# Optimization experiments

Measured on AMD Instinct MI355X. Metric: run time of the kernel, lower is better.

Reference implementation:

```python
import jax, jax.numpy as jnp
import numpy as np

HEADS = 20
DIM_HEAD = 64


def _bicubic_matrix(out_size, in_size, a=-0.75):
    """Separable torch-style bicubic (align_corners=False, antialias=False) as a [out,in] matrix."""
    W = np.zeros((out_size, in_size), dtype=np.float32)
    scale = in_size / out_size
    for i in range(out_size):
        x = (i + 0.5) * scale - 0.5
        x0 = int(np.floor(x))
        t = x - x0
        for tap, dist in zip(range(-1, 3), (1.0 + t, t, 1.0 - t, 2.0 - t)):
            d = abs(dist)
            if d <= 1.0:
                w = (a + 2.0) * d**3 - (a + 3.0) * d**2 + 1.0
            elif d < 2.0:
                w = a * d**3 - 5.0 * a * d**2 + 8.0 * a * d - 4.0 * a
            else:
                w = 0.0
            W[i, min(max(x0 + tap, 0), in_size - 1)] += w
    return jnp.asarray(W)


def setup_inputs() -> dict:
    key = jax.random.key(0)
    ks = jax.random.split(key, 8)
    B, N, QD, CD = 8, 4096, 1280, 1024
    inner = HEADS * DIM_HEAD
    return {
        "x": jax.random.normal(ks[0], (B, N, QD), dtype=jnp.float32),
        "context": jax.random.normal(ks[1], (B, 85, CD), dtype=jnp.float32),
        "Wq": jax.random.normal(ks[2], (QD, inner), dtype=jnp.float32) * 0.02,
        "Wk": jax.random.normal(ks[3], (CD, inner), dtype=jnp.float32) * 0.02,
        "Wv": jax.random.normal(ks[4], (CD, inner), dtype=jnp.float32) * 0.02,
        "Wo": jax.random.normal(ks[5], (inner, QD), dtype=jnp.float32) * 0.02,
        "bo": jnp.zeros((QD,), dtype=jnp.float32),
        "mask": jax.random.randint(ks[6], (B, 1, 256, 256), 0, 2, dtype=jnp.int32),
    }


def reference(x, context, Wq, Wk, Wv, Wo, bo, mask):
    B, N, _ = x.shape
    h, d = HEADS, DIM_HEAD
    scale = d ** -0.5
    q = (x @ Wq).reshape(B, N, h, d)
    k = (context @ Wk).reshape(B, -1, h, d)
    v = (context @ Wv).reshape(B, -1, h, d)
    # fp32 QK^T as in _ATTN_PRECISION == 'fp32'
    sim = jnp.einsum('bihd,bjhd->bhij', q.astype(jnp.float32), k.astype(jnp.float32)) * scale
    # build custom mask: bicubic-resize fg map to hw x hw, threshold, tile x4, append bg, prepend 77 ones
    hw = int(round(N ** 0.5))
    R = _bicubic_matrix(hw, mask.shape[-1])  # [hw, Hin]
    mf = mask.astype(jnp.float32)  # [B,1,H,W]
    resized = jnp.einsum('oh,bchw,pw->bcop', R, mf, R)  # [B,1,hw,hw]
    fg = (resized != 0).transpose(0, 2, 3, 1).reshape(B, hw * hw, 1)  # b (h w) c
    fg = jnp.repeat(fg, 4, axis=-1)  # b i (j k), k=4
    bg = ~fg
    base = jnp.ones((B, hw * hw, 77), dtype=bool)
    m = jnp.concatenate([base, fg, bg], axis=-1)  # [B, N, 85]
    neg = -jnp.finfo(sim.dtype).max
    sim = jnp.where(m[:, None, :, :], sim, neg)
    attn = jax.nn.softmax(sim, axis=-1)
    out = jnp.einsum('bhij,bjhd->bihd', attn.astype(v.dtype), v).reshape(B, N, h * d)
    return out @ Wo + bo
```

## Files before the change

kernel.cpp:

```cpp
#include <hip/hip_runtime.h>
#include <math.h>

typedef _Float16 f16;
typedef _Float16 half8 __attribute__((ext_vector_type(8)));
typedef _Float16 half4v __attribute__((ext_vector_type(4)));
typedef float f32x4 __attribute__((ext_vector_type(4)));

#define NB 8
#define SEQ 4096
#define QDIM 1280
#define CDIM 1024
#define INNER 1280
#define CTX 85
#define CTXP 96

#define VMCNT(n) asm volatile("s_waitcnt vmcnt(" #n ")" ::: "memory")
#define BAR() do { asm volatile("" ::: "memory"); __builtin_amdgcn_s_barrier(); asm volatile("" ::: "memory"); } while (0)

__device__ __forceinline__ void gload16(const void* g, void* l) {
  __builtin_amdgcn_global_load_lds(
      (const __attribute__((address_space(1))) unsigned int*)g,
      (__attribute__((address_space(3))) unsigned int*)l, 16, 0, 0);
}

__global__ void k_cast(const float* __restrict__ x, f16* __restrict__ xh, long n8) {
  long i = blockIdx.x * 256L + threadIdx.x;
  if (i >= n8) return;
  float4 a = ((const float4*)x)[2 * i];
  float4 b = ((const float4*)x)[2 * i + 1];
  half8 o;
  o[0] = (f16)a.x; o[1] = (f16)a.y; o[2] = (f16)a.z; o[3] = (f16)a.w;
  o[4] = (f16)b.x; o[5] = (f16)b.y; o[6] = (f16)b.z; o[7] = (f16)b.w;
  *(half8*)(xh + 8 * i) = o;
}

__global__ void k_castctx(const float* __restrict__ ctx, f16* __restrict__ ctxh) {
  int id = blockIdx.x * 256 + threadIdx.x;
  int b = id / (96 * 128);
  int rem = id % (96 * 128);
  int j = rem >> 7;
  int kc = (rem & 127) * 8;
  half8 o = {};
  if (j < CTX) {
    const float* p = ctx + ((long)b * CTX + j) * CDIM + kc;
    float4 a = *(const float4*)p;
    float4 c = *(const float4*)(p + 4);
    o[0] = (f16)a.x; o[1] = (f16)a.y; o[2] = (f16)a.z; o[3] = (f16)a.w;
    o[4] = (f16)c.x; o[5] = (f16)c.y; o[6] = (f16)c.z; o[7] = (f16)c.w;
  }
  *(half8*)(ctxh + (long)id * 8) = o;
}

__global__ __launch_bounds__(256) void k_transpose(const float* __restrict__ in,
                                                   f16* __restrict__ out, int K, int Nn) {
  __shared__ __attribute__((aligned(16))) f16 T[64][72];
  int n0 = blockIdx.x * 64, k0 = blockIdx.y * 64;
  int t = threadIdx.x;
  int kr = t >> 4, nc = (t & 15) * 4;
  for (int i = 0; i < 4; i++) {
    int k = kr + i * 16;
    float4 v = *(const float4*)&in[(long)(k0 + k) * Nn + n0 + nc];
    T[nc + 0][k] = (f16)v.x;
    T[nc + 1][k] = (f16)v.y;
    T[nc + 2][k] = (f16)v.z;
    T[nc + 3][k] = (f16)v.w;
  }
  __syncthreads();
  for (int i = 0; i < 2; i++) {
    int slot = t + i * 256;
    int n = slot >> 3, ch = (slot & 7) * 8;
    *(half8*)&out[(long)(n0 + n) * K + k0 + ch] = *(half8*)&T[n][ch];
  }
}

__global__ void k_fg(const int* __restrict__ mask, unsigned char* __restrict__ fg) {
  int id = blockIdx.x * 256 + threadIdx.x;
  int b = id >> 12, o = (id >> 6) & 63, p = id & 63;
  const int* mb = mask + (long)b * 65536;
  const int w[4] = {-3, 19, 19, -3};
  int s = 0;
  for (int dh = 0; dh < 4; dh++) {
    const int* row = mb + (4 * o + dh) * 256 + 4 * p;
    int rs = -3 * row[0] + 19 * row[1] + 19 * row[2] - 3 * row[3];
    s += w[dh] * rs;
  }
  fg[id] = (s != 0) ? 1 : 0;
}

__global__ __launch_bounds__(256) void k_kvproj(const f16* __restrict__ ctxh,
    const f16* __restrict__ WkT, const f16* __restrict__ WvT,
    f16* __restrict__ kpad, f16* __restrict__ vT) {
  int b = blockIdx.y, kv = blockIdx.z;
  const f16* WT = kv ? WvT : WkT;
  int w = threadIdx.x >> 6, lane = threadIdx.x & 63;
  int ln = lane & 15, qd = lane >> 4;
  int n0 = (blockIdx.x * 4 + w) * 16;
  const f16* arow = ctxh + ((long)b * CTXP + ln) * CDIM + qd * 8;
  const f16* brow = WT + (long)(n0 + ln) * CDIM + qd * 8;
  f32x4 acc[6] = {};
#pragma unroll 4
  for (int k0 = 0; k0 < CDIM; k0 += 32) {
    half8 bf = *(const half8*)(brow + k0);
#pragma unroll
    for (int mt = 0; mt < 6; mt++) {
      half8 af = *(const half8*)(arow + mt * 16 * CDIM + k0);
      acc[mt] = __builtin_amdgcn_mfma_f32_16x16x32_f16(af, bf, acc[mt], 0, 0, 0);
    }
  }
  if (kv == 0) {
    for (int mt = 0; mt < 6; mt++)
      for (int r = 0; r < 4; r++)
        kpad[((long)b * CTXP + mt * 16 + qd * 4 + r) * INNER + n0 + ln] = (f16)acc[mt][r];
  } else {
    for (int mt = 0; mt < 6; mt++) {
      half4v pv;
      for (int r = 0; r < 4; r++) pv[r] = (f16)acc[mt][r];
      *(half4v*)&vT[((long)b * INNER + n0 + ln) * CTXP + mt * 16 + qd * 4] = pv;
    }
  }
}

template <int OUT_F32>
__global__ __launch_bounds__(256) void k_gemm(const f16* __restrict__ A,
    const f16* __restrict__ Bt, const float* __restrict__ bias,
    f16* __restrict__ outh, float* __restrict__ outf, int K) {
  __shared__ __attribute__((aligned(16))) f16 Alds[128 * 64];
  __shared__ __attribute__((aligned(16))) f16 Blds[128 * 64];
  int tid = threadIdx.x, lane = tid & 63, w = tid >> 6;
  int wr = w >> 1, wc = w & 1;
  int ln = lane & 15, qd = lane >> 4;
  long m0 = (long)blockIdx.x * 128;
  int n0 = blockIdx.y * 128;
  int srow = lane >> 3;
  int schunk = lane & 7;
  f32x4 acc[4][4] = {};
  for (int k0 = 0; k0 < K; k0 += 64) {
#pragma unroll
    for (int i = 0; i < 4; i++) {
      int row = w * 32 + i * 8 + srow;
      int ca = (schunk ^ (row & 7)) * 8;
      gload16(&A[(m0 + row) * K + k0 + ca], &Alds[w * 2048 + i * 512]);
      gload16(&Bt[(long)(n0 + row) * K + k0 + ca], &Blds[w * 2048 + i * 512]);
    }
    __syncthreads();
#pragma unroll
    for (int s = 0; s < 2; s++) {
      half8 af[4], bf[4];
#pragma unroll
      for (int mt = 0; mt < 4; mt++) {
        int row = wr * 64 + mt * 16 + ln;
        af[mt] = *(half8*)&Alds[row * 64 + (((s * 4 + qd) ^ (row & 7)) * 8)];
      }
#pragma unroll
      for (int nt = 0; nt < 4; nt++) {
        int row = wc * 64 + nt * 16 + ln;
        bf[nt] = *(half8*)&Blds[row * 64 + (((s * 4 + qd) ^ (row & 7)) * 8)];
      }
#pragma unroll
      for (int mt = 0; mt < 4; mt++)
#pragma unroll
        for (int nt = 0; nt < 4; nt++)
          acc[mt][nt] = __builtin_amdgcn_mfma_f32_16x16x32_f16(af[mt], bf[nt], acc[mt][nt], 0, 0, 0);
    }
    __syncthreads();
  }
  for (int mt = 0; mt < 4; mt++) {
    long mrow = m0 + wr * 64 + mt * 16 + qd * 4;
    for (int nt = 0; nt < 4; nt++) {
      int n = n0 + wc * 64 + nt * 16 + ln;
      float bv = OUT_F32 ? bias[n] : 0.f;
      for (int r = 0; r < 4; r++) {
        if (OUT_F32) outf[(mrow + r) * INNER + n] = acc[mt][nt][r] + bv;
        else         outh[(mrow + r) * INNER + n] = (f16)acc[mt][nt][r];
      }
    }
  }
}

__device__ __forceinline__ void stage2(const f16* __restrict__ g, int ldK,
                                       f16* lds, int tid, int c0) {
#pragma unroll
  for (int c = c0; c < c0 + 2; ++c) {
    int row = c * 64 + (tid >> 3);
    int sc = (tid & 7) ^ (row & 7);
    gload16(g + (long)row * ldK + sc * 8, lds + c * 4096 + (tid >> 6) * 512);
  }
}

template <int OUT_F32>
__global__ __launch_bounds__(512, 2) void k_gemm256(const f16* __restrict__ A,
    const f16* __restrict__ Bt, const float* __restrict__ bias,
    f16* __restrict__ outh, float* __restrict__ outf, int K) {
  extern __shared__ __attribute__((aligned(16))) f16 smem[];
  f16* As0 = smem;
  f16* As1 = smem + 16384;
  f16* Bs0 = smem + 32768;
  f16* Bs1 = smem + 49152;
  const int NT = K >> 6;
  int tid = threadIdx.x, lane = tid & 63, w = tid >> 6;
  int wr = w >> 2, wc = w & 3;
  int ln = lane & 15, qd = lane >> 4;
  int wrb = wr * 128, wcb = wc * 64;
  int cpx = gridDim.x >> 3;
  int swz = (blockIdx.x & 7) * cpx + (blockIdx.x >> 3);
  int mtile = swz & 127, ntile = swz >> 7;
  long m0 = (long)mtile * 256;
  int n0 = ntile * 256;
  const f16* Ab = A + m0 * K;
  const f16* Bb = Bt + (long)n0 * K;

  half8 af[4][2], bf[2][2];
  f32x4 acc[8][4] = {};

  auto rdA = [&](const f16* Ac, int mh) {
#pragma unroll
    for (int mt = 0; mt < 4; ++mt) {
      int R = wrb + mh * 64 + mt * 16 + ln;
      const f16* rp = Ac + R * 64;
      int r7 = (R & 7) << 3;
      af[mt][0] = *(const half8*)(rp + ((qd << 3) ^ r7));
      af[mt][1] = *(const half8*)(rp + (((4 + qd) << 3) ^ r7));
    }
  };
  auto rdB = [&](const f16* Bc, int nh) {
#pragma unroll
    for (int nt = 0; nt < 2; ++nt) {
      int R = wcb + nh * 32 + nt * 16 + ln;
      const f16* rp = Bc + R * 64;
      int r7 = (R & 7) << 3;
      bf[nt][0] = *(const half8*)(rp + ((qd << 3) ^ r7));
      bf[nt][1] = *(const half8*)(rp + (((4 + qd) << 3) ^ r7));
    }
  };
  auto mm = [&](int mh, int nh) {
    __builtin_amdgcn_s_setprio(1);
#pragma unroll
    for (int ks = 0; ks < 2; ++ks)
#pragma unroll
      for (int mt = 0; mt < 4; ++mt)
#pragma unroll
        for (int nt = 0; nt < 2; ++nt)
          acc[mh * 4 + mt][nh * 2 + nt] = __builtin_amdgcn_mfma_f32_16x16x32_f16(
              af[mt][ks], bf[nt][ks], acc[mh * 4 + mt][nh * 2 + nt], 0, 0, 0);
    __builtin_amdgcn_s_setprio(0);
  };

  stage2(Ab, K, As0, tid, 0); stage2(Ab, K, As0, tid, 2);
  stage2(Bb, K, Bs0, tid, 0); stage2(Bb, K, Bs0, tid, 2);
  if (NT > 1) { stage2(Ab + 64, K, As1, tid, 0); VMCNT(2); } else { VMCNT(0); }
  BAR();

#define TILE256(KT, AC, BC, AN, BN_) do {                                        \
    rdA(AC, 0); rdB(BC, 0);                                                      \
    if ((KT) + 1 < NT) { stage2(Ab + ((KT) + 1) * 64, K, AN, tid, 2);            \
                         stage2(Bb + ((KT) + 1) * 64, K, BN_, tid, 0); }         \
    BAR(); mm(0, 0); BAR();                                                      \
    rdB(BC, 1);                                                                  \
    if ((KT) + 1 < NT) stage2(Bb + ((KT) + 1) * 64, K, BN_, tid, 2);             \
    BAR(); mm(0, 1); BAR();                                                      \
    rdA(AC, 1);                                                                  \
    BAR(); mm(1, 1); BAR();                                                      \
    rdB(BC, 0);                                                                  \
    if ((KT) + 2 < NT) stage2(Ab + ((KT) + 2) * 64, K, AC, tid, 0);              \
    BAR(); mm(1, 0);                                                             \
    if ((KT) + 2 < NT) { VMCNT(2); } else if ((KT) + 1 < NT) { VMCNT(0); }       \
    BAR();                                                                       \
  } while (0)

#pragma unroll 1
  for (int kt = 0; kt < NT; kt += 2) {
    TILE256(kt, As0, Bs0, As1, Bs1);
    TILE256(kt + 1, As1, Bs1, As0, Bs0);
  }
#undef TILE256

#pragma unroll
  for (int mt = 0; mt < 8; ++mt) {
    long rb = m0 + wrb + mt * 16 + qd * 4;
#pragma unroll
    for (int nt = 0; nt < 4; ++nt) {
      int col = n0 + wcb + nt * 16 + ln;
      if (OUT_F32) {
        float bv = bias[col];
#pragma unroll
        for (int r = 0; r < 4; ++r)
          outf[(rb + r) * INNER + col] = acc[mt][nt][r] + bv;
      } else {
#pragma unroll
        for (int r = 0; r < 4; ++r)
          outh[(rb + r) * INNER + col] = (f16)acc[mt][nt][r];
      }
    }
  }
}

__global__ __launch_bounds__(256) void k_attn(const f16* __restrict__ q,
    const f16* __restrict__ kpad, const f16* __restrict__ vT,
    const unsigned char* __restrict__ fg, f16* __restrict__ ao) {
  int mb = blockIdx.x;
  int h = blockIdx.y;
  int b = blockIdx.z;
  __shared__ __attribute__((aligned(16))) f16 Klds[CTXP][72];
  __shared__ __attribute__((aligned(16))) f16 Vlds[64][104];
  __shared__ __attribute__((aligned(16))) f16 Plds[4][16][104];
  int tid = threadIdx.x, lane = tid & 63, w = tid >> 6;
  int ln = lane & 15, qd = lane >> 4;

  for (int c = tid; c < CTXP * 8; c += 256) {
    int j = c >> 3, kc = (c & 7) * 8;
    *(half8*)&Klds[j][kc] = *(const half8*)&kpad[((long)b * CTXP + j) * INNER + h * 64 + kc];
  }
  for (int c = tid; c < 64 * 12; c += 256) {
    int d = c / 12, jc = (c % 12) * 8;
    *(half8*)&Vlds[d][jc] = *(const half8*)&vT[((long)b * INNER + h * 64 + d) * CTXP + jc];
  }
  __syncthreads();

  long mg = (long)b * SEQ + mb * 64 + w * 16 + ln;
  half8 qf[2];
  for (int s = 0; s < 2; s++)
    qf[s] = *(const half8*)&q[mg * INNER + h * 64 + s * 32 + qd * 8];

  f32x4 sacc[6] = {};
  for (int s = 0; s < 2; s++)
    for (int nt = 0; nt < 6; nt++) {
      half8 bf = *(half8*)&Klds[nt * 16 + ln][s * 32 + qd * 8];
      sacc[nt] = __builtin_amdgcn_mfma_f32_16x16x32_f16(qf[s], bf, sacc[nt], 0, 0, 0);
    }

  unsigned int fgw = *(const unsigned int*)&fg[(long)b * SEQ + mb * 64 + w * 16 + qd * 4];
  const float scale = 0.125f;
  for (int r = 0; r < 4; r++) {
    bool f = ((fgw >> (8 * r)) & 0xff) != 0;
    float vals[6];
    bool oks[6];
    float mx = -1e30f;
    for (int nt = 0; nt < 6; nt++) {
      int j = nt * 16 + ln;
      bool ok = (j < 77) || (j < 81 ? f : (j < 85 ? !f : false));
      float v = sacc[nt][r] * scale;
      vals[nt] = v; oks[nt] = ok;
      if (ok) mx = fmaxf(mx, v);
    }
    for (int d = 1; d < 16; d <<= 1) mx = fmaxf(mx, __shfl_xor(mx, d, 64));
    float sum = 0.f, p[6];
    for (int nt = 0; nt < 6; nt++) {
      p[nt] = oks[nt] ? __expf(vals[nt] - mx) : 0.f;
      sum += p[nt];
    }
    for (int d = 1; d < 16; d <<= 1) sum += __shfl_xor(sum, d, 64);
    float inv = 1.f / sum;
    for (int nt = 0; nt < 6; nt++)
      Plds[w][qd * 4 + r][nt * 16 + ln] = (f16)(p[nt] * inv);
  }
  __syncthreads();

  f32x4 oacc[4] = {};
  for (int ks = 0; ks < 3; ks++) {
    half8 pf = *(half8*)&Plds[w][ln][ks * 32 + qd * 8];
    for (int ntd = 0; ntd < 4; ntd++) {
      half8 vf = *(half8*)&Vlds[ntd * 16 + ln][ks * 32 + qd * 8];
      oacc[ntd] = __builtin_amdgcn_mfma_f32_16x16x32_f16(pf, vf, oacc[ntd], 0, 0, 0);
    }
  }
  for (int ntd = 0; ntd < 4; ntd++)
    for (int r = 0; r < 4; r++)
      Plds[w][qd * 4 + r][ntd * 16 + ln] = (f16)oacc[ntd][r];
  __syncthreads();
  long rowbase = (long)b * SEQ + mb * 64 + w * 16;
  for (int i = 0; i < 2; i++) {
    int slot = lane + i * 64;
    int rrow = slot >> 3, ch = (slot & 7) * 8;
    *(half8*)&ao[(rowbase + rrow) * INNER + h * 64 + ch] = *(half8*)&Plds[w][rrow][ch];
  }
}

extern "C" void kernel_launch(void* const* d_in, const int* in_sizes, int n_in,
                              void* d_out, int out_size, void* d_ws, size_t ws_size,
                              hipStream_t stream) {
  const float* x   = (const float*)d_in[0];
  const float* ctx = (const float*)d_in[1];
  const float* Wq  = (const float*)d_in[2];
  const float* Wk  = (const float*)d_in[3];
  const float* Wv  = (const float*)d_in[4];
  const float* Wo  = (const float*)d_in[5];
  const float* bo  = (const float*)d_in[6];
  const int*  mask = (const int*)d_in[7];
  float* out = (float*)d_out;

  char* ws = (char*)d_ws;
  size_t off = 0;
  f16* xh  = (f16*)(ws + off); off += 83886080;
  f16* q   = (f16*)(ws + off); off += 83886080;
  f16* ao  = (f16*)(ws + off); off += 83886080;
  f16* WqT = (f16*)(ws + off); off += 3276800;
  f16* WoT = (f16*)(ws + off); off += 3276800;
  f16* WkT = (f16*)(ws + off); off += 2621440;
  f16* WvT = (f16*)(ws + off); off += 2621440;
  f16* kpad= (f16*)(ws + off); off += 1966080;
  f16* vT  = (f16*)(ws + off); off += 1966080;
  f16* ctxh= (f16*)(ws + off); off += 1572864;
  unsigned char* fg = (unsigned char*)(ws + off); off += 32768;
  if (ws_size < off) return;

  static int g_use256 = -1;
  if (g_use256 < 0) {
    auto* f0 = k_gemm256<0>;
    auto* f1 = k_gemm256<1>;
    hipError_t e0 = hipFuncSetAttribute(reinterpret_cast<const void*>(f0),
                                        hipFuncAttributeMaxDynamicSharedMemorySize, 131072);
    hipError_t e1 = hipFuncSetAttribute(reinterpret_cast<const void*>(f1),
                                        hipFuncAttributeMaxDynamicSharedMemorySize, 131072);
    g_use256 = (e0 == hipSuccess && e1 == hipSuccess) ? 1 : 0;
  }

  k_cast<<<20480, 256, 0, stream>>>(x, xh, 5242880);
  k_castctx<<<384, 256, 0, stream>>>(ctx, ctxh);
  k_transpose<<<dim3(1280/64, 1280/64), 256, 0, stream>>>(Wq, WqT, 1280, 1280);
  k_transpose<<<dim3(1280/64, 1024/64), 256, 0, stream>>>(Wk, WkT, 1024, 1280);
  k_transpose<<<dim3(1280/64, 1024/64), 256, 0, stream>>>(Wv, WvT, 1024, 1280);
  k_transpose<<<dim3(1280/64, 1280/64), 256, 0, stream>>>(Wo, WoT, 1280, 1280);
  k_fg<<<128, 256, 0, stream>>>(mask, fg);
  k_kvproj<<<dim3(20, 8, 2), 256, 0, stream>>>(ctxh, WkT, WvT, kpad, vT);
  if (g_use256) {
    k_gemm256<0><<<640, 512, 131072, stream>>>(xh, WqT, nullptr, q, nullptr, 1280);
  } else {
    k_gemm<0><<<dim3(256, 10), 256, 0, stream>>>(xh, WqT, nullptr, q, nullptr, 1280);
  }
  k_attn<<<dim3(64, 20, 8), 256, 0, stream>>>(q, kpad, vT, fg, ao);
  if (g_use256) {
    k_gemm256<1><<<640, 512, 131072, stream>>>(ao, WoT, bo, nullptr, out, 1280);
  } else {
    k_gemm<1><<<dim3(256, 10), 256, 0, stream>>>(ao, WoT, bo, nullptr, out, 1280);
  }
}
```

Before: 680.4 us.

## Replace 256x256 double-buffered GEMM with 128x256 triple-buffered pipeline

Swaps the 256x256-tile, double-buffered GEMM, which needs many barriers per k-step, for a 128x256-tile kernel with three LDS slabs. Each k-step prefetches two steps ahead and uses a single barrier. The aim is fewer synchronisation stalls, better overlap of global-to-LDS loads with MFMA work, and twice as many blocks, which eases wave quantisation. In exchange each tile reuses loaded data less, and the larger LDS footprint (144 KB) still allows only one block per CU.

Measured after the change: 702.4 us. +3.2%, slower.

```diff
diff --git a/kernel.cpp b/kernel.cpp
--- a/kernel.cpp
+++ b/kernel.cpp
@@ -177,105 +177,96 @@
   }
 }
 
-__device__ __forceinline__ void stage2(const f16* __restrict__ g, int ldK,
-                                       f16* lds, int tid, int c0) {
-#pragma unroll
-  for (int c = c0; c < c0 + 2; ++c) {
+#define SLAB 24576
+
+__device__ __forceinline__ void stageA(const f16* __restrict__ g, int K, f16* lds, int tid) {
+#pragma unroll
+  for (int c = 0; c < 2; ++c) {
     int row = c * 64 + (tid >> 3);
     int sc = (tid & 7) ^ (row & 7);
-    gload16(g + (long)row * ldK + sc * 8, lds + c * 4096 + (tid >> 6) * 512);
+    gload16(g + (long)row * K + sc * 8, lds + c * 4096 + (tid >> 6) * 512);
+  }
+}
+__device__ __forceinline__ void stageB(const f16* __restrict__ g, int K, f16* lds, int tid) {
+#pragma unroll
+  for (int c = 0; c < 4; ++c) {
+    int row = c * 64 + (tid >> 3);
+    int sc = (tid & 7) ^ (row & 7);
+    gload16(g + (long)row * K + sc * 8, lds + c * 4096 + (tid >> 6) * 512);
   }
 }
 
 template <int OUT_F32>
-__global__ __launch_bounds__(512, 2) void k_gemm256(const f16* __restrict__ A,
+__global__ __launch_bounds__(512, 2) void k_gemm3(const f16* __restrict__ A,
     const f16* __restrict__ Bt, const float* __restrict__ bias,
     f16* __restrict__ outh, float* __restrict__ outf, int K) {
   extern __shared__ __attribute__((aligned(16))) f16 smem[];
-  f16* As0 = smem;
-  f16* As1 = smem + 16384;
-  f16* Bs0 = smem + 32768;
-  f16* Bs1 = smem + 49152;
   const int NT = K >> 6;
   int tid = threadIdx.x, lane = tid & 63, w = tid >> 6;
   int wr = w >> 2, wc = w & 3;
   int ln = lane & 15, qd = lane >> 4;
-  int wrb = wr * 128, wcb = wc * 64;
+  int wrb = wr * 64, wcb = wc * 64;
   int cpx = gridDim.x >> 3;
   int swz = (blockIdx.x & 7) * cpx + (blockIdx.x >> 3);
-  int mtile = swz & 127, ntile = swz >> 7;
-  long m0 = (long)mtile * 256;
+  int mtile = swz & 255, ntile = swz >> 8;
+  long m0 = (long)mtile * 128;
   int n0 = ntile * 256;
   const f16* Ab = A + m0 * K;
   const f16* Bb = Bt + (long)n0 * K;
 
-  half8 af[4][2], bf[2][2];
-  f32x4 acc[8][4] = {};
-
-  auto rdA = [&](const f16* Ac, int mh) {
+  f16* sl0 = smem;
+  f16* sl1 = smem + SLAB;
+  f16* sl2 = smem + 2 * SLAB;
+
+  half8 af[4][2], bf[4][2];
+  f32x4 acc[4][4] = {};
+
+  stageA(Ab, K, sl0, tid); stageB(Bb, K, sl0 + 8192, tid);
+  stageA(Ab + 64, K, sl1, tid); stageB(Bb + 64, K, sl1 + 8192, tid);
+  VMCNT(6);
+  BAR();
+
+  f16 *Cur = sl0, *Nx1 = sl1, *Nx2 = sl2;
+#pragma unroll 1
+  for (int kt = 0; kt < NT; ++kt) {
+    if (kt + 2 < NT) {
+      stageA(Ab + (kt + 2) * 64, K, Nx2, tid);
+      stageB(Bb + (kt + 2) * 64, K, Nx2 + 8192, tid);
+    }
 #pragma unroll
     for (int mt = 0; mt < 4; ++mt) {
-      int R = wrb + mh * 64 + mt * 16 + ln;
-      const f16* rp = Ac + R * 64;
+      int R = wrb + mt * 16 + ln;
+      const f16* rp = Cur + R * 64;
       int r7 = (R & 7) << 3;
       af[mt][0] = *(const half8*)(rp + ((qd << 3) ^ r7));
       af[mt][1] = *(const half8*)(rp + (((4 + qd) << 3) ^ r7));
     }
-  };
-  auto rdB = [&](const f16* Bc, int nh) {
-#pragma unroll
-    for (int nt = 0; nt < 2; ++nt) {
-      int R = wcb + nh * 32 + nt * 16 + ln;
-      const f16* rp = Bc + R * 64;
+#pragma unroll
+    for (int nt = 0; nt < 4; ++nt) {
+      int R = wcb + nt * 16 + ln;
+      const f16* rp = Cur + 8192 + R * 64;
       int r7 = (R & 7) << 3;
       bf[nt][0] = *(const half8*)(rp + ((qd << 3) ^ r7));
       bf[nt][1] = *(const half8*)(rp + (((4 + qd) << 3) ^ r7));
     }
-  };
-  auto mm = [&](int mh, int nh) {
     __builtin_amdgcn_s_setprio(1);
 #pragma unroll
     for (int ks = 0; ks < 2; ++ks)
 #pragma unroll
       for (int mt = 0; mt < 4; ++mt)
 #pragma unroll
-        for (int nt = 0; nt < 2; ++nt)
-          acc[mh * 4 + mt][nh * 2 + nt] = __builtin_amdgcn_mfma_f32_16x16x32_f16(
-              af[mt][ks], bf[nt][ks], acc[mh * 4 + mt][nh * 2 + nt], 0, 0, 0);
+        for (int nt = 0; nt < 4; ++nt)
+          acc[mt][nt] = __builtin_amdgcn_mfma_f32_16x16x32_f16(
+              af[mt][ks], bf[nt][ks], acc[mt][nt], 0, 0, 0);
     __builtin_amdgcn_s_setprio(0);
-  };
-
-  stage2(Ab, K, As0, tid, 0); stage2(Ab, K, As0, tid, 2);
-  stage2(Bb, K, Bs0, tid, 0); stage2(Bb, K, Bs0, tid, 2);
-  if (NT > 1) { stage2(Ab + 64, K, As1, tid, 0); VMCNT(2); } else { VMCNT(0); }
-  BAR();
-
-#define TILE256(KT, AC, BC, AN, BN_) do {                                        \
-    rdA(AC, 0); rdB(BC, 0);                                                      \
-    if ((KT) + 1 < NT) { stage2(Ab + ((KT) + 1) * 64, K, AN, tid, 2);            \
-                         stage2(Bb + ((KT) + 1) * 64, K, BN_, tid, 0); }         \
-    BAR(); mm(0, 0); BAR();                                                      \
-    rdB(BC, 1);                                                                  \
-    if ((KT) + 1 < NT) stage2(Bb + ((KT) + 1) * 64, K, BN_, tid, 2);             \
-    BAR(); mm(0, 1); BAR();                                                      \
-    rdA(AC, 1);                                                                  \
-    BAR(); mm(1, 1); BAR();                                                      \
-    rdB(BC, 0);                                                                  \
-    if ((KT) + 2 < NT) stage2(Ab + ((KT) + 2) * 64, K, AC, tid, 0);              \
-    BAR(); mm(1, 0);                                                             \
-    if ((KT) + 2 < NT) { VMCNT(2); } else if ((KT) + 1 < NT) { VMCNT(0); }       \
-    BAR();                                                                       \
-  } while (0)
-
-#pragma unroll 1
-  for (int kt = 0; kt < NT; kt += 2) {
-    TILE256(kt, As0, Bs0, As1, Bs1);
-    TILE256(kt + 1, As1, Bs1, As0, Bs0);
-  }
-#undef TILE256
-
-#pragma unroll
-  for (int mt = 0; mt < 8; ++mt) {
+    if (kt + 2 < NT) { VMCNT(6); }
+    else if (kt + 1 < NT) { VMCNT(0); }
+    BAR();
+    f16* t = Cur; Cur = Nx1; Nx1 = Nx2; Nx2 = t;
+  }
+
+#pragma unroll
+  for (int mt = 0; mt < 4; ++mt) {
     long rb = m0 + wrb + mt * 16 + qd * 4;
 #pragma unroll
     for (int nt = 0; nt < 4; ++nt) {
@@ -403,15 +394,15 @@
   unsigned char* fg = (unsigned char*)(ws + off); off += 32768;
   if (ws_size < off) return;
 
-  static int g_use256 = -1;
-  if (g_use256 < 0) {
-    auto* f0 = k_gemm256<0>;
-    auto* f1 = k_gemm256<1>;
+  static int g_use3 = -1;
+  if (g_use3 < 0) {
+    auto* f0 = k_gemm3<0>;
+    auto* f1 = k_gemm3<1>;
     hipError_t e0 = hipFuncSetAttribute(reinterpret_cast<const void*>(f0),
-                                        hipFuncAttributeMaxDynamicSharedMemorySize, 131072);
+                                        hipFuncAttributeMaxDynamicSharedMemorySize, 147456);
     hipError_t e1 = hipFuncSetAttribute(reinterpret_cast<const void*>(f1),
-                                        hipFuncAttributeMaxDynamicSharedMemorySize, 131072);
-    g_use256 = (e0 == hipSuccess && e1 == hipSuccess) ? 1 : 0;
+                                        hipFuncAttributeMaxDynamicSharedMemorySize, 147456);
+    g_use3 = (e0 == hipSuccess && e1 == hipSuccess) ? 1 : 0;
   }
 
   k_cast<<<20480, 256, 0, stream>>>(x, xh, 5242880);
@@ -422,14 +413,14 @@
   k_transpose<<<dim3(1280/64, 1280/64), 256, 0, stream>>>(Wo, WoT, 1280, 1280);
   k_fg<<<128, 256, 0, stream>>>(mask, fg);
   k_kvproj<<<dim3(20, 8, 2), 256, 0, stream>>>(ctxh, WkT, WvT, kpad, vT);
-  if (g_use256) {
-    k_gemm256<0><<<640, 512, 131072, stream>>>(xh, WqT, nullptr, q, nullptr, 1280);
+  if (g_use3) {
+    k_gemm3<0><<<1280, 512, 147456, stream>>>(xh, WqT, nullptr, q, nullptr, 1280);
   } else {
     k_gemm<0><<<dim3(256, 10), 256, 0, stream>>>(xh, WqT, nullptr, q, nullptr, 1280);
   }
   k_attn<<<dim3(64, 20, 8), 256, 0, stream>>>(q, kpad, vT, fg, ao);
-  if (g_use256) {
-    k_gemm256<1><<<640, 512, 131072, stream>>>(ao, WoT, bo, nullptr, out, 1280);
+  if (g_use3) {
+    k_gemm3<1><<<1280, 512, 147456, stream>>>(ao, WoT, bo, nullptr, out, 1280);
   } else {
     k_gemm<1><<<dim3(256, 10), 256, 0, stream>>>(ao, WoT, bo, nullptr, out, 1280);
   }
```
